# Kernel optimization log

Measured on AMD Instinct MI355X. Metric: run time of the kernel, lower is better.

The kernel has to match this reference:

```python
import jax, jax.numpy as jnp
import numpy as np

N_NODES = 50000
N_EDGES = 800000


def _spmm(edge_row, edge_col, edge_w, h):
    # sparse adj @ h via gather + segment-sum: adj[r,c] = edge_w
    msgs = edge_w[:, None] * h[edge_col]          # [E, D] gather
    return jax.ops.segment_sum(msgs, edge_row, num_segments=N_NODES)


def setup_inputs() -> dict:
    key = jax.random.key(0)
    ks = jax.random.split(key, 8)
    x = jax.random.normal(ks[0], (N_NODES, 256), dtype=jnp.float32)
    edge_row = jax.random.randint(ks[1], (N_EDGES,), 0, N_NODES, dtype=jnp.int32)
    edge_col = jax.random.randint(ks[2], (N_EDGES,), 0, N_NODES, dtype=jnp.int32)
    edge_w = jax.random.uniform(ks[3], (N_EDGES,), dtype=jnp.float32)
    W1 = jax.random.normal(ks[4], (256, 128), dtype=jnp.float32) * 0.06
    b1 = jnp.zeros((128,), dtype=jnp.float32)
    W2 = jax.random.normal(ks[5], (128, 32), dtype=jnp.float32) * 0.09
    b2 = jnp.zeros((32,), dtype=jnp.float32)
    return {"x": x, "edge_row": edge_row, "edge_col": edge_col,
            "edge_w": edge_w, "W1": W1, "b1": b1, "W2": W2, "b2": b2}


def reference(x, edge_row, edge_col, edge_w, W1, b1, W2, b2):
    # Layer 1: support = X @ W1 ; out = relu(A @ support + b1)
    # (dropout is identity in eval mode)
    h = jax.nn.relu(_spmm(edge_row, edge_col, edge_w, x @ W1) + b1)
    # Layer 2
    out = jax.nn.relu(_spmm(edge_row, edge_col, edge_w, h @ W2) + b2)
    return out
```

## Files before the change

### kernel.cpp

```cpp
#include <hip/hip_runtime.h>

#define N_NODES 50000
#define N_EDGES 800000
#define D0 256
#define D1 128
#define D2 32
#define CAP 64
#define NB 391
#define BCAP 3072
#define EB 8192
#define SC_BLOCKS 98
#define G1_BLOCKS 782

typedef unsigned short u16;
typedef unsigned int   u32;
typedef unsigned long long u64;
typedef __attribute__((ext_vector_type(8))) short bf16x8;
typedef __attribute__((ext_vector_type(4))) float f32x4;

__device__ inline u32 bf16rne(float f) {
    union { float f; u32 u; } c; c.f = f;
    return (c.u + 0x7FFFu + ((c.u >> 16) & 1u)) >> 16;
}
__device__ inline float bfhi(u32 v) {
    union { u32 u; float f; } c; c.u = v & 0xFFFF0000u; return c.f;
}
__device__ inline float bflo(u32 v) {
    union { u32 u; float f; } c; c.u = v << 16; return c.f;
}

__global__ __launch_bounds__(256) void front_kernel(const float* __restrict__ W1,
                                                    u16* __restrict__ Bsw1,
                                                    const float* __restrict__ W2,
                                                    u16* __restrict__ Bsw2) {
    const int bid = blockIdx.x;
    if (bid < 16) {
        const int id = bid * 256 + threadIdx.x;
        const int lane = id & 63;
        const int t    = (id >> 6) & 7;
        const int ks   = id >> 9;
        const int n     = t * 16 + (lane & 15);
        const int kbase = ks * 32 + (lane >> 4) * 8;
        u32 v[8];
        #pragma unroll
        for (int j = 0; j < 8; ++j) v[j] = bf16rne(W1[(kbase + j) * D1 + n]);
        uint4 w;
        w.x = v[0] | (v[1] << 16);
        w.y = v[2] | (v[3] << 16);
        w.z = v[4] | (v[5] << 16);
        w.w = v[6] | (v[7] << 16);
        ((uint4*)Bsw1)[id] = w;
    } else {
        const int id = (bid - 16) * 256 + threadIdx.x;
        const int lane = id & 63;
        const int t    = (id >> 6) & 1;
        const int ks   = id >> 7;
        const int n     = t * 16 + (lane & 15);
        const int kbase = ks * 32 + (lane >> 4) * 8;
        u32 v[8];
        #pragma unroll
        for (int j = 0; j < 8; ++j) v[j] = bf16rne(W2[(kbase + j) * D2 + n]);
        uint4 w;
        w.x = v[0] | (v[1] << 16);
        w.y = v[2] | (v[3] << 16);
        w.z = v[4] | (v[5] << 16);
        w.w = v[6] | (v[7] << 16);
        ((uint4*)Bsw2)[id] = w;
    }
}

__global__ __launch_bounds__(1024) void scatter_kernel(const int* __restrict__ erow,
                                                       const int* __restrict__ ecol,
                                                       const float* __restrict__ ew,
                                                       u32* __restrict__ bcur,
                                                       u64* __restrict__ ebuf) {
    __shared__ u32 hist[NB];
    __shared__ u32 lbase[NB];
    const int tid = threadIdx.x;
    if (tid < NB) hist[tid] = 0;
    __syncthreads();
    const int ebase = blockIdx.x * EB;
    #pragma unroll
    for (int k = 0; k < EB / 1024; ++k) {
        const int e = ebase + k * 1024 + tid;
        if (e < N_EDGES) atomicAdd(&hist[erow[e] >> 7], 1u);
    }
    __syncthreads();
    if (tid < NB) {
        const u32 h = hist[tid];
        lbase[tid] = h ? atomicAdd(&bcur[tid], h) : 0u;
        hist[tid] = 0;
    }
    __syncthreads();
    #pragma unroll
    for (int k = 0; k < EB / 1024; ++k) {
        const int e = ebase + k * 1024 + tid;
        if (e < N_EDGES) {
            const int r = erow[e];
            const int c = ecol[e];
            const float w = ew[e];
            const int b = r >> 7;
            const u32 lr = atomicAdd(&hist[b], 1u);
            const u32 pos = lbase[b] + lr;
            if (pos < BCAP)
                ebuf[(size_t)b * BCAP + pos] =
                    (u64)(u32)c | ((u64)(u32)(r & 127) << 16) | ((u64)bf16rne(w) << 32);
        }
    }
}

__global__ __launch_bounds__(256) void gb_kernel(const float* __restrict__ x,
                                                 const u16* __restrict__ Bsw1,
                                                 u16* __restrict__ s1b,
                                                 const u32* __restrict__ bcur,
                                                 const u64* __restrict__ ebuf,
                                                 int* __restrict__ cnt,
                                                 u32* __restrict__ eg) {
    __shared__ u32 seg[128 * CAP];
    __shared__ u32 lcnt[128];
    const int bid = blockIdx.x;
    if (bid < NB) {
        const int b = bid;
        for (int i = threadIdx.x; i < 128; i += 256) lcnt[i] = 0;
        __syncthreads();
        int n = (int)bcur[b];
        if (n > BCAP) n = BCAP;
        const u64* ep = ebuf + (size_t)b * BCAP;
        for (int i = threadIdx.x; i < n; i += 256) {
            const u64 e = ep[i];
            const u32 c  = (u32)(e & 0xFFFFu);
            const u32 lr = (u32)((e >> 16) & 0x7Fu);
            const u32 w  = (u32)(e >> 32);
            const u32 p = atomicAdd(&lcnt[lr], 1u);
            if (p < CAP)
                seg[lr * CAP + p] = c | (w << 16);
        }
        __syncthreads();
        const int rows = min(128, N_NODES - b * 128);
        for (int i = threadIdx.x; i < rows; i += 256)
            cnt[b * 128 + i] = (int)min(lcnt[i], (u32)CAP);
        u32* dst = eg + (size_t)b * 128 * CAP;
        const int nvec = rows * (CAP / 4);
        for (int i = threadIdx.x; i < nvec; i += 256)
            ((uint4*)dst)[i] = ((const uint4*)seg)[i];
    } else {
        const int gb   = bid - NB;
        const int lane = threadIdx.x & 63;
        const int wave = threadIdx.x >> 6;
        const int rowbase = gb * 64 + wave * 16;
        const int m    = lane & 15;
        const int quad = lane >> 4;
        int arow = rowbase + m;
        if (arow >= N_NODES) arow = N_NODES - 1;
        const float* aptr = x + (size_t)arow * D0 + quad * 8;

        f32x4 acc[8];
        #pragma unroll
        for (int t = 0; t < 8; ++t) acc[t] = (f32x4){0.f, 0.f, 0.f, 0.f};

        #pragma unroll
        for (int ks = 0; ks < 8; ++ks) {
            const float4 f0 = *(const float4*)(aptr + ks * 32);
            const float4 f1 = *(const float4*)(aptr + ks * 32 + 4);
            bf16x8 a;
            a[0] = (short)bf16rne(f0.x); a[1] = (short)bf16rne(f0.y);
            a[2] = (short)bf16rne(f0.z); a[3] = (short)bf16rne(f0.w);
            a[4] = (short)bf16rne(f1.x); a[5] = (short)bf16rne(f1.y);
            a[6] = (short)bf16rne(f1.z); a[7] = (short)bf16rne(f1.w);
            const u16* bp = Bsw1 + ((size_t)(ks * 8) * 64 + lane) * 8;
            #pragma unroll
            for (int t = 0; t < 8; ++t) {
                const bf16x8 b = *(const bf16x8*)(bp + (size_t)t * 64 * 8);
                acc[t] = __builtin_amdgcn_mfma_f32_16x16x32_bf16(a, b, acc[t], 0, 0, 0);
            }
        }
        const int orow = rowbase + quad * 4;
        #pragma unroll
        for (int r = 0; r < 4; ++r) {
            const int row = orow + r;
            if (row < N_NODES) {
                u16* op = s1b + (size_t)row * D1 + m;
                #pragma unroll
                for (int t = 0; t < 8; ++t) op[t * 16] = (u16)bf16rne(acc[t][r]);
            }
        }
    }
}

__global__ __launch_bounds__(256) void spmm_csr128_kernel(const int* __restrict__ cnt,
                                                          const u32* __restrict__ eg,
                                                          const u16* __restrict__ src,
                                                          const float* __restrict__ bias,
                                                          u16* __restrict__ dst) {
    const int lane = threadIdx.x;
    const int row  = blockIdx.x * 8 + threadIdx.y;
    if (row >= N_NODES) return;
    int len = cnt[row];
    if (len > CAP) len = CAP;
    const u32* ep = eg + (size_t)row * CAP;
    float4 a0 = {0.f,0.f,0.f,0.f}, a1 = {0.f,0.f,0.f,0.f};
    float4 a2 = {0.f,0.f,0.f,0.f}, a3 = {0.f,0.f,0.f,0.f};
    int j = 0;
    for (; j + 3 < len; j += 4) {
        const uint4 e4 = *(const uint4*)(ep + j);
        const uint2 v0 = ((const uint2*)(src + (size_t)(e4.x & 0xFFFFu) * D1))[lane];
        const uint2 v1 = ((const uint2*)(src + (size_t)(e4.y & 0xFFFFu) * D1))[lane];
        const uint2 v2 = ((const uint2*)(src + (size_t)(e4.z & 0xFFFFu) * D1))[lane];
        const uint2 v3 = ((const uint2*)(src + (size_t)(e4.w & 0xFFFFu) * D1))[lane];
        const float w0 = bfhi(e4.x), w1 = bfhi(e4.y), w2 = bfhi(e4.z), w3 = bfhi(e4.w);
        a0.x += w0 * bflo(v0.x); a0.y += w0 * bfhi(v0.x);
        a0.z += w0 * bflo(v0.y); a0.w += w0 * bfhi(v0.y);
        a1.x += w1 * bflo(v1.x); a1.y += w1 * bfhi(v1.x);
        a1.z += w1 * bflo(v1.y); a1.w += w1 * bfhi(v1.y);
        a2.x += w2 * bflo(v2.x); a2.y += w2 * bfhi(v2.x);
        a2.z += w2 * bflo(v2.y); a2.w += w2 * bfhi(v2.y);
        a3.x += w3 * bflo(v3.x); a3.y += w3 * bfhi(v3.x);
        a3.z += w3 * bflo(v3.y); a3.w += w3 * bfhi(v3.y);
    }
    for (; j < len; ++j) {
        const u32 e0 = ep[j];
        const float w0 = bfhi(e0);
        const uint2 v0 = ((const uint2*)(src + (size_t)(e0 & 0xFFFFu) * D1))[lane];
        a0.x += w0 * bflo(v0.x); a0.y += w0 * bfhi(v0.x);
        a0.z += w0 * bflo(v0.y); a0.w += w0 * bfhi(v0.y);
    }
    const float4 b4 = ((const float4*)bias)[lane];
    float rx = a0.x + a1.x + a2.x + a3.x + b4.x; rx = rx > 0.f ? rx : 0.f;
    float ry = a0.y + a1.y + a2.y + a3.y + b4.y; ry = ry > 0.f ? ry : 0.f;
    float rz = a0.z + a1.z + a2.z + a3.z + b4.z; rz = rz > 0.f ? rz : 0.f;
    float rw = a0.w + a1.w + a2.w + a3.w + b4.w; rw = rw > 0.f ? rw : 0.f;
    uint2 o;
    o.x = bf16rne(rx) | (bf16rne(ry) << 16);
    o.y = bf16rne(rz) | (bf16rne(rw) << 16);
    ((uint2*)(dst + (size_t)row * D1))[lane] = o;
}

__global__ __launch_bounds__(256) void gemm2_mfma_kernel(const u16* __restrict__ hb,
                                                         const u16* __restrict__ Bsw2,
                                                         u16* __restrict__ s2b) {
    const int lane = threadIdx.x & 63;
    const int wave = threadIdx.x >> 6;
    const int rowbase = blockIdx.x * 64 + wave * 16;
    const int m    = lane & 15;
    const int quad = lane >> 4;
    int arow = rowbase + m;
    if (arow >= N_NODES) arow = N_NODES - 1;
    const u16* aptr = hb + (size_t)arow * D1 + quad * 8;

    f32x4 acc0 = (f32x4){0.f,0.f,0.f,0.f};
    f32x4 acc1 = (f32x4){0.f,0.f,0.f,0.f};

    #pragma unroll
    for (int ks = 0; ks < 4; ++ks) {
        const bf16x8 a = *(const bf16x8*)(aptr + ks * 32);
        const u16* bp = Bsw2 + ((size_t)(ks * 2) * 64 + lane) * 8;
        const bf16x8 b0 = *(const bf16x8*)(bp);
        const bf16x8 b1 = *(const bf16x8*)(bp + (size_t)64 * 8);
        acc0 = __builtin_amdgcn_mfma_f32_16x16x32_bf16(a, b0, acc0, 0, 0, 0);
        acc1 = __builtin_amdgcn_mfma_f32_16x16x32_bf16(a, b1, acc1, 0, 0, 0);
    }
    const int orow = rowbase + quad * 4;
    #pragma unroll
    for (int r = 0; r < 4; ++r) {
        const int row = orow + r;
        if (row < N_NODES) {
            u16* op = s2b + (size_t)row * D2 + m;
            op[0]  = (u16)bf16rne(acc0[r]);
            op[16] = (u16)bf16rne(acc1[r]);
        }
    }
}

__global__ __launch_bounds__(256) void spmm_csr32_kernel(const int* __restrict__ cnt,
                                                         const u32* __restrict__ eg,
                                                         const u16* __restrict__ src,
                                                         const float* __restrict__ bias,
                                                         float* __restrict__ out) {
    const int lane = threadIdx.x;
    const int row  = blockIdx.x * 16 + threadIdx.y;
    if (row >= N_NODES) return;
    int len = cnt[row];
    if (len > CAP) len = CAP;
    const u32* ep = eg + (size_t)row * CAP;
    float ax0=0.f, ay0=0.f, ax1=0.f, ay1=0.f, ax2=0.f, ay2=0.f, ax3=0.f, ay3=0.f;
    int j = 0;
    for (; j + 3 < len; j += 4) {
        const uint4 e4 = *(const uint4*)(ep + j);
        const u32 v0 = ((const u32*)(src + (size_t)(e4.x & 0xFFFFu) * D2))[lane];
        const u32 v1 = ((const u32*)(src + (size_t)(e4.y & 0xFFFFu) * D2))[lane];
        const u32 v2 = ((const u32*)(src + (size_t)(e4.z & 0xFFFFu) * D2))[lane];
        const u32 v3 = ((const u32*)(src + (size_t)(e4.w & 0xFFFFu) * D2))[lane];
        const float w0 = bfhi(e4.x), w1 = bfhi(e4.y), w2 = bfhi(e4.z), w3 = bfhi(e4.w);
        ax0 += w0 * bflo(v0); ay0 += w0 * bfhi(v0);
        ax1 += w1 * bflo(v1); ay1 += w1 * bfhi(v1);
        ax2 += w2 * bflo(v2); ay2 += w2 * bfhi(v2);
        ax3 += w3 * bflo(v3); ay3 += w3 * bfhi(v3);
    }
    for (; j < len; ++j) {
        const u32 e0 = ep[j];
        const u32 v0 = ((const u32*)(src + (size_t)(e0 & 0xFFFFu) * D2))[lane];
        const float w0 = bfhi(e0);
        ax0 += w0 * bflo(v0); ay0 += w0 * bfhi(v0);
    }
    const float2 b2v = ((const float2*)bias)[lane];
    float vx = ax0 + ax1 + ax2 + ax3 + b2v.x; vx = vx > 0.f ? vx : 0.f;
    float vy = ay0 + ay1 + ay2 + ay3 + b2v.y; vy = vy > 0.f ? vy : 0.f;
    ((float2*)(out + (size_t)row * D2))[lane] = make_float2(vx, vy);
}

extern "C" void kernel_launch(void* const* d_in, const int* in_sizes, int n_in,
                              void* d_out, int out_size, void* d_ws, size_t ws_size,
                              hipStream_t stream) {
    const float* x    = (const float*)d_in[0];
    const int*   erow = (const int*)  d_in[1];
    const int*   ecol = (const int*)  d_in[2];
    const float* ew   = (const float*)d_in[3];
    const float* W1   = (const float*)d_in[4];
    const float* b1   = (const float*)d_in[5];
    const float* W2   = (const float*)d_in[6];
    const float* b2   = (const float*)d_in[7];
    float* out = (float*)d_out;

    int* cnt   = (int*)d_ws;
    u32* bcur  = (u32*)(cnt + N_NODES);
    u32* eg    = (u32*)(bcur + 512);
    u16* Bsw1  = (u16*)(eg + (size_t)N_NODES * CAP);
    u16* Bsw2  = Bsw1 + 8 * 8 * 64 * 8;
    u16* s1b   = Bsw2 + 4 * 2 * 64 * 8;
    u16* hb    = s1b + (size_t)N_NODES * D1;
    u16* s2b   = hb + (size_t)N_NODES * D1;
    u64* ebuf  = (u64*)hb;

    hipMemsetAsync(bcur, 0, 512 * sizeof(u32), stream);
    front_kernel<<<18, 256, 0, stream>>>(W1, Bsw1, W2, Bsw2);
    scatter_kernel<<<SC_BLOCKS, 1024, 0, stream>>>(erow, ecol, ew, bcur, ebuf);
    gb_kernel<<<NB + G1_BLOCKS, 256, 0, stream>>>(x, Bsw1, s1b, bcur, ebuf, cnt, eg);
    spmm_csr128_kernel<<<(N_NODES + 7) / 8, dim3(32, 8), 0, stream>>>(cnt, eg, s1b, b1, hb);
    gemm2_mfma_kernel<<<(N_NODES + 63) / 64, 256, 0, stream>>>(hb, Bsw2, s2b);
    spmm_csr32_kernel<<<(N_NODES + 15) / 16, dim3(16, 16), 0, stream>>>(cnt, eg, s2b, b2, out);
}
```

Baseline: 195.2 us.

## Slice layer-1 SpMM by feature columns, merge front into scatter, shrink CAP

Splits the layer-1 sparse aggregation into 8 feature slices handled by separate blocks so each gather touches a narrower column range. Merges the weight-swizzle kernel into the scatter launch to drop a launch, reduces the per-row edge capacity to 48, and adds 8-way unrolled gather loops in both SpMM kernels. Risks include repeated reading of edge indices per slice, narrower per-lane loads, and truncation of rows with more than 48 edges.

```diff
diff --git a/kernel.cpp b/kernel.cpp
--- a/kernel.cpp
+++ b/kernel.cpp
@@ -5,12 +5,14 @@
 #define D0 256
 #define D1 128
 #define D2 32
-#define CAP 64
+#define CAP 48
 #define NB 391
 #define BCAP 3072
 #define EB 8192
 #define SC_BLOCKS 98
+#define SW_BLOCKS 4
 #define G1_BLOCKS 782
+#define RG_BLOCKS 1563
 
 typedef unsigned short u16;
 typedef unsigned int   u32;
@@ -29,13 +31,51 @@
     union { u32 u; float f; } c; c.u = v << 16; return c.f;
 }
 
-__global__ __launch_bounds__(256) void front_kernel(const float* __restrict__ W1,
-                                                    u16* __restrict__ Bsw1,
-                                                    const float* __restrict__ W2,
-                                                    u16* __restrict__ Bsw2) {
-    const int bid = blockIdx.x;
-    if (bid < 16) {
-        const int id = bid * 256 + threadIdx.x;
+__global__ __launch_bounds__(1024) void scatter_kernel(const int* __restrict__ erow,
+                                                       const int* __restrict__ ecol,
+                                                       const float* __restrict__ ew,
+                                                       u32* __restrict__ bcur,
+                                                       u64* __restrict__ ebuf,
+                                                       const float* __restrict__ W1,
+                                                       u16* __restrict__ Bsw1,
+                                                       const float* __restrict__ W2,
+                                                       u16* __restrict__ Bsw2) {
+    __shared__ u32 hist[NB];
+    __shared__ u32 lbase[NB];
+    const int tid = threadIdx.x;
+    if (blockIdx.x < SC_BLOCKS) {
+        if (tid < NB) hist[tid] = 0;
+        __syncthreads();
+        const int ebase = blockIdx.x * EB;
+        #pragma unroll
+        for (int k = 0; k < EB / 1024; ++k) {
+            const int e = ebase + k * 1024 + tid;
+            if (e < N_EDGES) atomicAdd(&hist[erow[e] >> 7], 1u);
+        }
+        __syncthreads();
+        if (tid < NB) {
+            const u32 h = hist[tid];
+            lbase[tid] = h ? atomicAdd(&bcur[tid], h) : 0u;
+            hist[tid] = 0;
+        }
+        __syncthreads();
+        #pragma unroll
+        for (int k = 0; k < EB / 1024; ++k) {
+            const int e = ebase + k * 1024 + tid;
+            if (e < N_EDGES) {
+                const int r = erow[e];
+                const int c = ecol[e];
+                const float w = ew[e];
+                const int b = r >> 7;
+                const u32 lr = atomicAdd(&hist[b], 1u);
+                const u32 pos = lbase[b] + lr;
+                if (pos < BCAP)
+                    ebuf[(size_t)b * BCAP + pos] =
+                        (u64)(u32)c | ((u64)(u32)(r & 127) << 16) | ((u64)bf16rne(w) << 32);
+            }
+        }
+    } else if (blockIdx.x < SC_BLOCKS + SW_BLOCKS) {
+        const int id = (blockIdx.x - SC_BLOCKS) * 1024 + tid;
         const int lane = id & 63;
         const int t    = (id >> 6) & 7;
         const int ks   = id >> 9;
@@ -50,8 +90,8 @@
         w.z = v[4] | (v[5] << 16);
         w.w = v[6] | (v[7] << 16);
         ((uint4*)Bsw1)[id] = w;
-    } else {
-        const int id = (bid - 16) * 256 + threadIdx.x;
+    } else if (tid < 512) {
+        const int id = tid;
         const int lane = id & 63;
         const int t    = (id >> 6) & 1;
         const int ks   = id >> 7;
@@ -66,46 +106,6 @@
         w.z = v[4] | (v[5] << 16);
         w.w = v[6] | (v[7] << 16);
         ((uint4*)Bsw2)[id] = w;
-    }
-}
-
-__global__ __launch_bounds__(1024) void scatter_kernel(const int* __restrict__ erow,
-                                                       const int* __restrict__ ecol,
-                                                       const float* __restrict__ ew,
-                                                       u32* __restrict__ bcur,
-                                                       u64* __restrict__ ebuf) {
-    __shared__ u32 hist[NB];
-    __shared__ u32 lbase[NB];
-    const int tid = threadIdx.x;
-    if (tid < NB) hist[tid] = 0;
-    __syncthreads();
-    const int ebase = blockIdx.x * EB;
-    #pragma unroll
-    for (int k = 0; k < EB / 1024; ++k) {
-        const int e = ebase + k * 1024 + tid;
-        if (e < N_EDGES) atomicAdd(&hist[erow[e] >> 7], 1u);
-    }
-    __syncthreads();
-    if (tid < NB) {
-        const u32 h = hist[tid];
-        lbase[tid] = h ? atomicAdd(&bcur[tid], h) : 0u;
-        hist[tid] = 0;
-    }
-    __syncthreads();
-    #pragma unroll
-    for (int k = 0; k < EB / 1024; ++k) {
-        const int e = ebase + k * 1024 + tid;
-        if (e < N_EDGES) {
-            const int r = erow[e];
-            const int c = ecol[e];
-            const float w = ew[e];
-            const int b = r >> 7;
-            const u32 lr = atomicAdd(&hist[b], 1u);
-            const u32 pos = lbase[b] + lr;
-            if (pos < BCAP)
-                ebuf[(size_t)b * BCAP + pos] =
-                    (u64)(u32)c | ((u64)(u32)(r & 127) << 16) | ((u64)bf16rne(w) << 32);
-        }
     }
 }
 
@@ -187,52 +187,66 @@
     }
 }
 
-__global__ __launch_bounds__(256) void spmm_csr128_kernel(const int* __restrict__ cnt,
+__global__ __launch_bounds__(256) void spmm1_slice_kernel(const int* __restrict__ cnt,
                                                           const u32* __restrict__ eg,
                                                           const u16* __restrict__ src,
-                                                          const float* __restrict__ bias,
-                                                          u16* __restrict__ dst) {
-    const int lane = threadIdx.x;
-    const int row  = blockIdx.x * 8 + threadIdx.y;
+                                                          const float* __restrict__ b1,
+                                                          u16* __restrict__ hb) {
+    const int tx = threadIdx.x;
+    const int s  = blockIdx.x & 7;
+    const int rg = blockIdx.x >> 3;
+    const int row = rg * 32 + threadIdx.y;
     if (row >= N_NODES) return;
     int len = cnt[row];
     if (len > CAP) len = CAP;
     const u32* ep = eg + (size_t)row * CAP;
-    float4 a0 = {0.f,0.f,0.f,0.f}, a1 = {0.f,0.f,0.f,0.f};
-    float4 a2 = {0.f,0.f,0.f,0.f}, a3 = {0.f,0.f,0.f,0.f};
+    const u16* sp = src + s * 16;
+    float ax0=0.f, ay0=0.f, ax1=0.f, ay1=0.f, ax2=0.f, ay2=0.f, ax3=0.f, ay3=0.f;
     int j = 0;
+    for (; j + 7 < len; j += 8) {
+        const uint4 e4a = *(const uint4*)(ep + j);
+        const uint4 e4b = *(const uint4*)(ep + j + 4);
+        const u32 v0 = ((const u32*)(sp + (size_t)(e4a.x & 0xFFFFu) * D1))[tx];
+        const u32 v1 = ((const u32*)(sp + (size_t)(e4a.y & 0xFFFFu) * D1))[tx];
+        const u32 v2 = ((const u32*)(sp + (size_t)(e4a.z & 0xFFFFu) * D1))[tx];
+        const u32 v3 = ((const u32*)(sp + (size_t)(e4a.w & 0xFFFFu) * D1))[tx];
+        const u32 v4 = ((const u32*)(sp + (size_t)(e4b.x & 0xFFFFu) * D1))[tx];
+        const u32 v5 = ((const u32*)(sp + (size_t)(e4b.y & 0xFFFFu) * D1))[tx];
+        const u32 v6 = ((const u32*)(sp + (size_t)(e4b.z & 0xFFFFu) * D1))[tx];
+        const u32 v7 = ((const u32*)(sp + (size_t)(e4b.w & 0xFFFFu) * D1))[tx];
+        const float w0 = bfhi(e4a.x), w1 = bfhi(e4a.y), w2 = bfhi(e4a.z), w3 = bfhi(e4a.w);
+        const float w4 = bfhi(e4b.x), w5 = bfhi(e4b.y), w6 = bfhi(e4b.z), w7 = bfhi(e4b.w);
+        ax0 += w0 * bflo(v0); ay0 += w0 * bfhi(v0);
+        ax1 += w1 * bflo(v1); ay1 += w1 * bfhi(v1);
+        ax2 += w2 * bflo(v2); ay2 += w2 * bfhi(v2);
+        ax3 += w3 * bflo(v3); ay3 += w3 * bfhi(v3);
+        ax0 += w4 * bflo(v4); ay0 += w4 * bfhi(v4);
+        ax1 += w5 * bflo(v5); ay1 += w5 * bfhi(v5);
+        ax2 += w6 * bflo(v6); ay2 += w6 * bfhi(v6);
+        ax3 += w7 * bflo(v7); ay3 += w7 * bfhi(v7);
+    }
     for (; j + 3 < len; j += 4) {
         const uint4 e4 = *(const uint4*)(ep + j);
-        const uint2 v0 = ((const uint2*)(src + (size_t)(e4.x & 0xFFFFu) * D1))[lane];
-        const uint2 v1 = ((const uint2*)(src + (size_t)(e4.y & 0xFFFFu) * D1))[lane];
-        const uint2 v2 = ((const uint2*)(src + (size_t)(e4.z & 0xFFFFu) * D1))[lane];
-        const uint2 v3 = ((const uint2*)(src + (size_t)(e4.w & 0xFFFFu) * D1))[lane];
+        const u32 v0 = ((const u32*)(sp + (size_t)(e4.x & 0xFFFFu) * D1))[tx];
+        const u32 v1 = ((const u32*)(sp + (size_t)(e4.y & 0xFFFFu) * D1))[tx];
+        const u32 v2 = ((const u32*)(sp + (size_t)(e4.z & 0xFFFFu) * D1))[tx];
+        const u32 v3 = ((const u32*)(sp + (size_t)(e4.w & 0xFFFFu) * D1))[tx];
         const float w0 = bfhi(e4.x), w1 = bfhi(e4.y), w2 = bfhi(e4.z), w3 = bfhi(e4.w);
-        a0.x += w0 * bflo(v0.x); a0.y += w0 * bfhi(v0.x);
-        a0.z += w0 * bflo(v0.y); a0.w += w0 * bfhi(v0.y);
-        a1.x += w1 * bflo(v1.x); a1.y += w1 * bfhi(v1.x);
-        a1.z += w1 * bflo(v1.y); a1.w += w1 * bfhi(v1.y);
-        a2.x += w2 * bflo(v2.x); a2.y += w2 * bfhi(v2.x);
-        a2.z += w2 * bflo(v2.y); a2.w += w2 * bfhi(v2.y);
-        a3.x += w3 * bflo(v3.x); a3.y += w3 * bfhi(v3.x);
-        a3.z += w3 * bflo(v3.y); a3.w += w3 * bfhi(v3.y);
+        ax0 += w0 * bflo(v0); ay0 += w0 * bfhi(v0);
+        ax1 += w1 * bflo(v1); ay1 += w1 * bfhi(v1);
+        ax2 += w2 * bflo(v2); ay2 += w2 * bfhi(v2);
+        ax3 += w3 * bflo(v3); ay3 += w3 * bfhi(v3);
     }
     for (; j < len; ++j) {
         const u32 e0 = ep[j];
+        const u32 v0 = ((const u32*)(sp + (size_t)(e0 & 0xFFFFu) * D1))[tx];
         const float w0 = bfhi(e0);
-        const uint2 v0 = ((const uint2*)(src + (size_t)(e0 & 0xFFFFu) * D1))[lane];
-        a0.x += w0 * bflo(v0.x); a0.y += w0 * bfhi(v0.x);
-        a0.z += w0 * bflo(v0.y); a0.w += w0 * bfhi(v0.y);
-    }
-    const float4 b4 = ((const float4*)bias)[lane];
-    float rx = a0.x + a1.x + a2.x + a3.x + b4.x; rx = rx > 0.f ? rx : 0.f;
-    float ry = a0.y + a1.y + a2.y + a3.y + b4.y; ry = ry > 0.f ? ry : 0.f;
-    float rz = a0.z + a1.z + a2.z + a3.z + b4.z; rz = rz > 0.f ? rz : 0.f;
-    float rw = a0.w + a1.w + a2.w + a3.w + b4.w; rw = rw > 0.f ? rw : 0.f;
-    uint2 o;
-    o.x = bf16rne(rx) | (bf16rne(ry) << 16);
-    o.y = bf16rne(rz) | (bf16rne(rw) << 16);
-    ((uint2*)(dst + (size_t)row * D1))[lane] = o;
+        ax0 += w0 * bflo(v0); ay0 += w0 * bfhi(v0);
+    }
+    const float2 bv = ((const float2*)(b1 + s * 16))[tx];
+    float vx = ax0 + ax1 + ax2 + ax3 + bv.x; vx = vx > 0.f ? vx : 0.f;
+    float vy = ay0 + ay1 + ay2 + ay3 + bv.y; vy = vy > 0.f ? vy : 0.f;
+    ((u32*)(hb + (size_t)row * D1 + s * 16))[tx] = bf16rne(vx) | (bf16rne(vy) << 16);
 }
 
 __global__ __launch_bounds__(256) void gemm2_mfma_kernel(const u16* __restrict__ hb,
@@ -284,6 +298,28 @@
     const u32* ep = eg + (size_t)row * CAP;
     float ax0=0.f, ay0=0.f, ax1=0.f, ay1=0.f, ax2=0.f, ay2=0.f, ax3=0.f, ay3=0.f;
     int j = 0;
+    for (; j + 7 < len; j += 8) {
+        const uint4 e4a = *(const uint4*)(ep + j);
+        const uint4 e4b = *(const uint4*)(ep + j + 4);
+        const u32 v0 = ((const u32*)(src + (size_t)(e4a.x & 0xFFFFu) * D2))[lane];
+        const u32 v1 = ((const u32*)(src + (size_t)(e4a.y & 0xFFFFu) * D2))[lane];
+        const u32 v2 = ((const u32*)(src + (size_t)(e4a.z & 0xFFFFu) * D2))[lane];
+        const u32 v3 = ((const u32*)(src + (size_t)(e4a.w & 0xFFFFu) * D2))[lane];
+        const u32 v4 = ((const u32*)(src + (size_t)(e4b.x & 0xFFFFu) * D2))[lane];
+        const u32 v5 = ((const u32*)(src + (size_t)(e4b.y & 0xFFFFu) * D2))[lane];
+        const u32 v6 = ((const u32*)(src + (size_t)(e4b.z & 0xFFFFu) * D2))[lane];
+        const u32 v7 = ((const u32*)(src + (size_t)(e4b.w & 0xFFFFu) * D2))[lane];
+        const float w0 = bfhi(e4a.x), w1 = bfhi(e4a.y), w2 = bfhi(e4a.z), w3 = bfhi(e4a.w);
+        const float w4 = bfhi(e4b.x), w5 = bfhi(e4b.y), w6 = bfhi(e4b.z), w7 = bfhi(e4b.w);
+        ax0 += w0 * bflo(v0); ay0 += w0 * bfhi(v0);
+        ax1 += w1 * bflo(v1); ay1 += w1 * bfhi(v1);
+        ax2 += w2 * bflo(v2); ay2 += w2 * bfhi(v2);
+        ax3 += w3 * bflo(v3); ay3 += w3 * bfhi(v3);
+        ax0 += w4 * bflo(v4); ay0 += w4 * bfhi(v4);
+        ax1 += w5 * bflo(v5); ay1 += w5 * bfhi(v5);
+        ax2 += w6 * bflo(v6); ay2 += w6 * bfhi(v6);
+        ax3 += w7 * bflo(v7); ay3 += w7 * bfhi(v7);
+    }
     for (; j + 3 < len; j += 4) {
         const uint4 e4 = *(const uint4*)(ep + j);
         const u32 v0 = ((const u32*)(src + (size_t)(e4.x & 0xFFFFu) * D2))[lane];
@@ -329,13 +365,13 @@
     u16* s1b   = Bsw2 + 4 * 2 * 64 * 8;
     u16* hb    = s1b + (size_t)N_NODES * D1;
     u16* s2b   = hb + (size_t)N_NODES * D1;
-    u64* ebuf  = (u64*)hb;
+    u64* ebuf  = (u64*)(s2b + (size_t)N_NODES * D2);
 
     hipMemsetAsync(bcur, 0, 512 * sizeof(u32), stream);
-    front_kernel<<<18, 256, 0, stream>>>(W1, Bsw1, W2, Bsw2);
-    scatter_kernel<<<SC_BLOCKS, 1024, 0, stream>>>(erow, ecol, ew, bcur, ebuf);
+    scatter_kernel<<<SC_BLOCKS + SW_BLOCKS + 1, 1024, 0, stream>>>(
+        erow, ecol, ew, bcur, ebuf, W1, Bsw1, W2, Bsw2);
     gb_kernel<<<NB + G1_BLOCKS, 256, 0, stream>>>(x, Bsw1, s1b, bcur, ebuf, cnt, eg);
-    spmm_csr128_kernel<<<(N_NODES + 7) / 8, dim3(32, 8), 0, stream>>>(cnt, eg, s1b, b1, hb);
+    spmm1_slice_kernel<<<RG_BLOCKS * 8, dim3(8, 32), 0, stream>>>(cnt, eg, s1b, b1, hb);
     gemm2_mfma_kernel<<<(N_NODES + 63) / 64, 256, 0, stream>>>(hb, Bsw2, s2b);
     spmm_csr32_kernel<<<(N_NODES + 15) / 16, dim3(16, 16), 0, stream>>>(cnt, eg, s2b, b2, out);
 }
```

After: 229.3 us. 17.5% more time.
